# Kernel optimization log

Hardware: AMD Instinct MI355X
Metric: run time of the kernel (lower is better)

Reference implementation:

```python
import jax, jax.numpy as jnp
import numpy as np

EPS = 1e-5
K = 20

def knn(x, k):
    # x: (B, 3, N) -> idx (B, N, k) of nearest neighbors (negative sq-dist topk)
    inner = -2.0 * jnp.einsum('bcn,bcm->bnm', x, x)
    xx = jnp.sum(x * x, axis=1)  # (B, N)
    pd = -xx[:, :, None] - inner - xx[:, None, :]
    return jax.lax.top_k(pd, k)[1]

def graph_feature(feats, idx):
    # feats: (B, C, N), idx: (B, N, k) -> (B, 2C, N, k)
    ft = jnp.transpose(feats, (0, 2, 1))  # (B, N, C)
    gathered = jax.vmap(lambda f, i: f[i])(ft, idx)  # (B, N, k, C)
    center = ft[:, :, None, :]  # (B, N, 1, C)
    out = jnp.concatenate([gathered - center,
                           jnp.broadcast_to(center, gathered.shape)], axis=3)
    return jnp.transpose(out, (0, 3, 1, 2))  # (B, 2C, N, k)

def bn2d(h, g, b):
    m = jnp.mean(h, axis=(0, 2, 3), keepdims=True)
    v = jnp.var(h, axis=(0, 2, 3), keepdims=True)
    return (h - m) * jax.lax.rsqrt(v + EPS) * g[None, :, None, None] + b[None, :, None, None]

def bn1d(h, g, b):
    m = jnp.mean(h, axis=(0, 2), keepdims=True)
    v = jnp.var(h, axis=(0, 2), keepdims=True)
    return (h - m) * jax.lax.rsqrt(v + EPS) * g[None, :, None] + b[None, :, None]

def edge_block(x, feats, w, g, b):
    idx = knn(x, K)
    ef = graph_feature(feats, idx)                  # (B, 2C, N, k)
    h = jnp.einsum('bcnk,oc->bonk', ef, w)          # 1x1 conv, no bias
    h = jnp.tanh(bn2d(h, g, b))
    return jnp.max(h, axis=-1)                      # (B, O, N)


def setup_inputs() -> dict:
    key = jax.random.key(0)
    ks = jax.random.split(key, 20)
    B, N, FD, EMB = 8, 2048, 3, 1024
    def w_init(k, o, i):
        return jax.random.normal(k, (o, i), dtype=jnp.float32) * (1.0 / np.sqrt(i))
    inp = {
        'x': jax.random.normal(ks[0], (B, N, 3), dtype=jnp.float32),
        'features': jax.random.normal(ks[1], (B, N, FD), dtype=jnp.float32),
        'w1': w_init(ks[2], 64, 2 * FD),
        'g1': jnp.ones((64,), jnp.float32), 'b1': jnp.zeros((64,), jnp.float32),
        'w2': w_init(ks[3], 64, 128),
        'g2': jnp.ones((64,), jnp.float32), 'b2': jnp.zeros((64,), jnp.float32),
        'w3': w_init(ks[4], 128, 128),
        'g3': jnp.ones((128,), jnp.float32), 'b3': jnp.zeros((128,), jnp.float32),
        'w4': w_init(ks[5], 256, 256),
        'g4': jnp.ones((256,), jnp.float32), 'b4': jnp.zeros((256,), jnp.float32),
        'w5': w_init(ks[6], EMB, 512),
        'g5': jnp.ones((EMB,), jnp.float32), 'b5': jnp.zeros((EMB,), jnp.float32),
    }
    return inp


def reference(x, features, w1, g1, b1, w2, g2, b2, w3, g3, b3, w4, g4, b4, w5, g5, b5):
    xt = jnp.transpose(x, (0, 2, 1))          # (B, 3, N)
    ft = jnp.transpose(features, (0, 2, 1))   # (B, FD, N)
    B = xt.shape[0]
    f1 = edge_block(xt, ft, w1, g1, b1)       # (B, 64, N)
    f2 = edge_block(xt, f1, w2, g2, b2)       # (B, 64, N)
    f3 = edge_block(xt, f2, w3, g3, b3)       # (B, 128, N)
    f4 = edge_block(xt, f3, w4, g4, b4)       # (B, 256, N)
    cat = jnp.concatenate([f1, f2, f3, f4], axis=1)   # (B, 512, N)
    f5 = jnp.tanh(bn1d(jnp.einsum('bcn,oc->bon', cat, w5), g5, b5))  # (B, EMB, N)
    mx = jnp.max(f5, axis=-1)
    av = jnp.mean(f5, axis=-1)
    return jnp.concatenate([mx, av], axis=1)  # (B, 2*EMB)
```

## Files before the change

kernel.cpp:

```cpp
#include <hip/hip_runtime.h>
#include <cstdio>
#include <cstdint>

#define NPTS 2048
#define NB   8
#define KK   20

typedef __attribute__((ext_vector_type(8))) short  short8;
typedef __attribute__((ext_vector_type(8))) unsigned short ushort8;
typedef __attribute__((ext_vector_type(4))) float  f32x4;
typedef unsigned short ushort;
typedef unsigned int   uint;

#define AS1 __attribute__((address_space(1)))
#define AS3 __attribute__((address_space(3)))

__device__ __forceinline__ ushort f2bf(float f) {
    uint u = __float_as_uint(f);
    u += 0x7fffu + ((u >> 16) & 1u);
    return (ushort)(u >> 16);
}
__device__ __forceinline__ float bf2f(ushort s) { return __uint_as_float((uint)s << 16); }

__device__ __forceinline__ void gload16(const ushort* g, ushort* l) {
    __builtin_amdgcn_global_load_lds((const AS1 uint*)(const void*)g,
                                     (AS3 uint*)(void*)l, 16, 0, 0);
}

__global__ __launch_bounds__(256) void knn_kernel(const float* __restrict__ x,
                                                  int* __restrict__ idx)
{
    __shared__ float4 sp[NPTS];
    const int tid = threadIdx.x;
    const int wv = tid >> 6, lane = tid & 63;
    const int gn0 = blockIdx.x * 4;
    const int b = gn0 >> 11;
    const float* xb = x + (size_t)b * NPTS * 3;

    for (int p = tid; p < NPTS; p += 256) {
        const float a0 = xb[p * 3 + 0], a1 = xb[p * 3 + 1], a2 = xb[p * 3 + 2];
        sp[p] = make_float4(a0, a1, a2, a0 * a0 + a1 * a1 + a2 * a2);
    }
    __syncthreads();

    const int n = (gn0 & (NPTS - 1)) + wv;
    const float4 pn = sp[n];
    const float xxn = pn.w;

    float d[32];
#pragma unroll
    for (int i = 0; i < 32; ++i) {
        const float4 pm = sp[lane + i * 64];
        const float dot = pm.x * pn.x + pm.y * pn.y + pm.z * pn.z;
        const float inner = -2.0f * dot;
        d[i] = (-xxn - inner) - pm.w;
    }

    int* op = idx + ((size_t)b * NPTS + n) * KK;
    for (int it = 0; it < KK; ++it) {
        float bv = -1e38f;
        int   bi = 0;
#pragma unroll
        for (int i = 0; i < 32; ++i) {
            const bool better = d[i] > bv;
            bv = better ? d[i] : bv;
            bi = better ? (lane + i * 64) : bi;
        }
#pragma unroll
        for (int s = 32; s; s >>= 1) {
            const float ov = __shfl_xor(bv, s);
            const int   oi = __shfl_xor(bi, s);
            const bool better = (ov > bv) || (ov == bv && oi < bi);
            bv = better ? ov : bv;
            bi = better ? oi : bi;
        }
        if (lane == 0) op[it] = bi;
#pragma unroll
        for (int i = 0; i < 32; ++i)
            if (bi == lane + i * 64) d[i] = -1e38f;
    }
}

__global__ __launch_bounds__(256) void y1_kernel(const float* __restrict__ feats,
                                                 const float* __restrict__ w1,
                                                 float* __restrict__ Y)
{
    __shared__ float w[384];
    const int tid = threadIdx.x;
    for (int i = tid; i < 384; i += 256) w[i] = w1[i];
    __syncthreads();

    const int b  = blockIdx.y;
    const int p  = blockIdx.x * 2 + (tid >> 7);
    const int o2 = tid & 127;
    const int o = o2 & 63, half = o2 >> 6;
    const float* fp = feats + ((size_t)b * NPTS + p) * 3;
    const float f0 = fp[0], f1 = fp[1], f2 = fp[2];
    const float* wr = &w[o * 6 + half * 3];
    Y[((size_t)b * NPTS + p) * 128 + o2] = wr[0] * f0 + wr[1] * f1 + wr[2] * f2;
}

__global__ __launch_bounds__(256) void wsplit_kernel(const float* __restrict__ w2,
                                                     const float* __restrict__ w3,
                                                     const float* __restrict__ w4,
                                                     ushort* q2h, ushort* q2l,
                                                     ushort* q3h, ushort* q3l,
                                                     ushort* q4h, ushort* q4l)
{
    const int t = blockIdx.x * 256 + threadIdx.x;
    float v; ushort *dh, *dl; int off;
    if (t < 8192)        { int i = t;         int m = i >> 6, c = i & 63;  int o = m & 63,  hf = m >> 6; v = w2[o * 128 + hf * 64  + c]; dh = q2h; dl = q2l; off = i; }
    else if (t < 24576)  { int i = t - 8192;  int m = i >> 6, c = i & 63;  int o = m & 127, hf = m >> 7; v = w3[o * 128 + hf * 64  + c]; dh = q3h; dl = q3l; off = i; }
    else if (t < 90112)  { int i = t - 24576; int m = i >> 7, c = i & 127; int o = m & 255, hf = m >> 8; v = w4[o * 256 + hf * 128 + c]; dh = q4h; dl = q4l; off = i; }
    else return;
    const ushort h = f2bf(v);
    dh[off] = h;
    dl[off] = f2bf(v - bf2f(h));
}

template<bool PF32>
__global__ __launch_bounds__(256) void gemm_mfma(const float* __restrict__ Pf,
                                                 const ushort* __restrict__ Ph,
                                                 const ushort* __restrict__ Pl,
                                                 const ushort* __restrict__ Qh,
                                                 const ushort* __restrict__ Ql,
                                                 float* __restrict__ Out,
                                                 int K, int pitchP, int pitchQ, int ldO,
                                                 long strideP, long strideQ, long strideO)
{
    constexpr int PH = 0, PL = 8192, QH = 16384, QL = 24576;
    __shared__ ushort lds_buf[32768];

    const int tid  = threadIdx.x;
    const int wv   = tid >> 6, lane = tid & 63;
    const int i0   = blockIdx.x * 128;
    const int j0   = blockIdx.y * 128;
    const long prow0 = (long)blockIdx.z * strideP + (long)i0 * pitchP;
    const long qrow0 = (long)blockIdx.z * strideQ + (long)j0 * pitchQ;

    const int iw = (wv >> 1) * 64;
    const int jw = (wv & 1) * 64;
    const int lr = lane & 15;
    const int lc = lane >> 4;

    f32x4 acc[4][4];
#pragma unroll
    for (int f = 0; f < 4; ++f)
#pragma unroll
        for (int g = 0; g < 4; ++g) acc[f][g] = (f32x4){0.f, 0.f, 0.f, 0.f};

    for (int k0 = 0; k0 < K; k0 += 64) {
        __syncthreads();
        {
            const int r8 = lane >> 3;
            const int cp = lane & 7;
#pragma unroll
            for (int q = 0; q < 4; ++q) {
                const int row = wv * 32 + q * 8 + r8;
                const int cl  = cp ^ (row & 7);
                const long go = (long)row * pitchQ + k0 + cl * 8;
                gload16(Qh + qrow0 + go, &lds_buf[QH + (wv * 32 + q * 8) * 64]);
                gload16(Ql + qrow0 + go, &lds_buf[QL + (wv * 32 + q * 8) * 64]);
            }
        }
        if constexpr (!PF32) {
            const int r8 = lane >> 3;
            const int cp = lane & 7;
#pragma unroll
            for (int q = 0; q < 4; ++q) {
                const int row = wv * 32 + q * 8 + r8;
                const int cl  = cp ^ (row & 7);
                const long go = (long)row * pitchP + k0 + cl * 8;
                gload16(Ph + prow0 + go, &lds_buf[PH + (wv * 32 + q * 8) * 64]);
                gload16(Pl + prow0 + go, &lds_buf[PL + (wv * 32 + q * 8) * 64]);
            }
        } else {
#pragma unroll
            for (int r = 0; r < 4; ++r) {
                const int id  = r * 256 + tid;
                const int row = id >> 3, cl = id & 7;
                const int cp  = cl ^ (row & 7);
                const float* gp = Pf + prow0 + (long)row * pitchP + k0 + cl * 8;
                const float4 v0 = *(const float4*)gp;
                const float4 v1 = *(const float4*)(gp + 4);
                const float vv[8] = {v0.x, v0.y, v0.z, v0.w, v1.x, v1.y, v1.z, v1.w};
                ushort8 hi, lo;
#pragma unroll
                for (int e2 = 0; e2 < 8; ++e2) {
                    const ushort h = f2bf(vv[e2]);
                    hi[e2] = h;
                    lo[e2] = f2bf(vv[e2] - bf2f(h));
                }
                *(ushort8*)&lds_buf[PH + row * 64 + cp * 8] = hi;
                *(ushort8*)&lds_buf[PL + row * 64 + cp * 8] = lo;
            }
        }
        asm volatile("s_waitcnt vmcnt(0)" ::: "memory");
        __syncthreads();

#pragma unroll
        for (int kk = 0; kk < 2; ++kk) {
            const int cpa = (kk * 4 + lc) ^ (lr & 7);
            short8 ah[4], al[4], bh[4], bl[4];
#pragma unroll
            for (int f = 0; f < 4; ++f) {
                const int ra = (iw + f * 16 + lr) * 64 + cpa * 8;
                ah[f] = *(const short8*)&lds_buf[PH + ra];
                al[f] = *(const short8*)&lds_buf[PL + ra];
                const int rb = (jw + f * 16 + lr) * 64 + cpa * 8;
                bh[f] = *(const short8*)&lds_buf[QH + rb];
                bl[f] = *(const short8*)&lds_buf[QL + rb];
            }
#pragma unroll
            for (int f = 0; f < 4; ++f)
#pragma unroll
                for (int g = 0; g < 4; ++g) {
                    acc[f][g] = __builtin_amdgcn_mfma_f32_16x16x32_bf16(ah[f], bh[g], acc[f][g], 0, 0, 0);
                    acc[f][g] = __builtin_amdgcn_mfma_f32_16x16x32_bf16(ah[f], bl[g], acc[f][g], 0, 0, 0);
                    acc[f][g] = __builtin_amdgcn_mfma_f32_16x16x32_bf16(al[f], bh[g], acc[f][g], 0, 0, 0);
                }
        }
    }

    const long ob = (long)blockIdx.z * strideO;
#pragma unroll
    for (int f = 0; f < 4; ++f) {
        const int i = i0 + iw + f * 16 + lc * 4;
#pragma unroll
        for (int g = 0; g < 4; ++g) {
            const int j = j0 + jw + g * 16 + lr;
#pragma unroll
            for (int r = 0; r < 4; ++r)
                Out[ob + (long)(i + r) * ldO + j] = acc[f][g][r];
        }
    }
}

template<int O, int NCH>
__global__ __launch_bounds__(256) void edge_apply(const float* __restrict__ Y,
                                                  const int* __restrict__ knn_idx,
                                                  float* __restrict__ mx_out,
                                                  double* __restrict__ st)
{
    constexpr int M = 2 * O;
    constexpr int NPB = 256 / O;
    const int b   = blockIdx.y;
    const int tid = threadIdx.x;
    const int o   = tid & (O - 1);
    const int sub = tid / O;
    const int n0  = blockIdx.x * (NPB * NCH);
    const size_t rowb = (size_t)b * NPTS;
    float s = 0.f, s2 = 0.f;

#pragma unroll
    for (int it = 0; it < NCH; ++it) {
        const int n = n0 + it * NPB + sub;
        const float* yr = Y + (rowb + n) * M;
        const float base = yr[O + o] - yr[o];
        const int* ip = knn_idx + (rowb + n) * KK;
        int mm[KK];
#pragma unroll
        for (int j = 0; j < KK; ++j) mm[j] = ip[j];
        float h[KK];
#pragma unroll
        for (int j = 0; j < KK; ++j) h[j] = Y[(rowb + mm[j]) * M + o];
        float mx = -1e38f;
#pragma unroll
        for (int j = 0; j < KK; ++j) {
            const float v = h[j] + base;
            mx = fmaxf(mx, v);
            s += v;
            s2 = fmaf(v, v, s2);
        }
        mx_out[(rowb + n) * O + o] = mx;
    }
    double* stp = st + (size_t)(blockIdx.x & 7) * (2 * O);
    atomicAdd(&stp[o],     (double)s);
    atomicAdd(&stp[O + o], (double)s2);
}

template<int O>
__global__ __launch_bounds__(256) void edge_finalize(const float* __restrict__ mx_in,
                                                     const double* __restrict__ st,
                                                     const float* __restrict__ gamma,
                                                     const float* __restrict__ beta,
                                                     ushort* __restrict__ ch,
                                                     ushort* __restrict__ cl_,
                                                     int c0)
{
    __shared__ float ssc[256], ssh[256];
    const int b = blockIdx.y;
    const int tid = threadIdx.x;
    if (tid < O) {
        double ssum = 0.0, s2sum = 0.0;
#pragma unroll
        for (int sl = 0; sl < 8; ++sl) {
            ssum  += st[(size_t)sl * (2 * O) + tid];
            s2sum += st[(size_t)sl * (2 * O) + O + tid];
        }
        const double cnt = (double)NB * NPTS * KK;
        const double mean = ssum / cnt;
        const double var  = s2sum / cnt - mean * mean;
        const float rs = rsqrtf((float)var + 1e-5f);
        const float sc = gamma[tid] * rs;
        ssc[tid] = sc;
        ssh[tid] = beta[tid] - (float)mean * sc;
    }
    __syncthreads();

    const int o   = tid & (O - 1);
    const int sub = tid / O;
    const int n0  = blockIdx.x * 8;
    constexpr int NPB = 256 / O;
#pragma unroll
    for (int it = 0; it < 8 / NPB; ++it) {
        const int n = n0 + it * NPB + sub;
        const float v = mx_in[((size_t)b * NPTS + n) * O + o];
        const float f = tanhf(fmaf(v, ssc[o], ssh[o]));
        const ushort h = f2bf(f);
        const size_t co = ((size_t)b * NPTS + n) * 512 + c0 + o;
        ch[co]  = h;
        cl_[co] = f2bf(f - bf2f(h));
    }
}

__global__ __launch_bounds__(256) void estats_kernel(const float* __restrict__ e,
                                                     double* __restrict__ st)
{
    const int o = blockIdx.x;
    const int tid = threadIdx.x;
    double s = 0.0, s2 = 0.0;
    for (int b = 0; b < NB; ++b) {
        const float* row = e + ((size_t)(b * 1024 + o)) * NPTS;
        for (int n = tid; n < NPTS; n += 256) {
            const float v = row[n];
            s  += v;
            s2 += (double)v * v;
        }
    }
    __shared__ double sh_s[4], sh_s2[4];
#pragma unroll
    for (int d = 32; d > 0; d >>= 1) { s += __shfl_xor(s, d); s2 += __shfl_xor(s2, d); }
    const int lane = tid & 63, wv = tid >> 6;
    if (lane == 0) { sh_s[wv] = s; sh_s2[wv] = s2; }
    __syncthreads();
    if (tid == 0) {
        st[o]        = sh_s[0] + sh_s[1] + sh_s[2] + sh_s[3];
        st[1024 + o] = sh_s2[0] + sh_s2[1] + sh_s2[2] + sh_s2[3];
    }
}

__global__ __launch_bounds__(256) void final_kernel(const float* __restrict__ e,
                                                    const double* __restrict__ st,
                                                    const float* __restrict__ g5,
                                                    const float* __restrict__ b5,
                                                    float* __restrict__ out)
{
    const int b = blockIdx.y;
    const int wv = threadIdx.x >> 6, lane = threadIdx.x & 63;
    const int o = blockIdx.x * 4 + wv;
    const double cnt = (double)NB * NPTS;
    const double mean = st[o] / cnt;
    const double var  = st[1024 + o] / cnt - mean * mean;
    const float rs = rsqrtf((float)var + 1e-5f);
    const float sc = g5[o] * rs;
    const float sh = b5[o] - (float)mean * sc;
    const float* row = e + ((size_t)(b * 1024 + o)) * NPTS;
    float mx = -1e38f, sm = 0.f;
    for (int n = lane; n < NPTS; n += 64) {
        const float v = tanhf(fmaf(row[n], sc, sh));
        mx = fmaxf(mx, v);
        sm += v;
    }
#pragma unroll
    for (int d = 32; d > 0; d >>= 1) {
        mx = fmaxf(mx, __shfl_xor(mx, d));
        sm += __shfl_xor(sm, d);
    }
    if (lane == 0) {
        out[(size_t)b * 2048 + o]        = mx;
        out[(size_t)b * 2048 + 1024 + o] = sm * (1.0f / 2048.0f);
    }
}

extern "C" void kernel_launch(void* const* d_in, const int* in_sizes, int n_in,
                              void* d_out, int out_size, void* d_ws, size_t ws_size,
                              hipStream_t stream)
{
    (void)in_sizes; (void)n_in; (void)out_size;
    const float* x  = (const float*)d_in[0];
    const float* ft = (const float*)d_in[1];
    const float* w1 = (const float*)d_in[2];
    const float* g1 = (const float*)d_in[3];
    const float* b1 = (const float*)d_in[4];
    const float* w2 = (const float*)d_in[5];
    const float* g2 = (const float*)d_in[6];
    const float* b2 = (const float*)d_in[7];
    const float* w3 = (const float*)d_in[8];
    const float* g3 = (const float*)d_in[9];
    const float* b3 = (const float*)d_in[10];
    const float* w4 = (const float*)d_in[11];
    const float* g4 = (const float*)d_in[12];
    const float* b4 = (const float*)d_in[13];
    const float* w5 = (const float*)d_in[14];
    const float* g5 = (const float*)d_in[15];
    const float* b5 = (const float*)d_in[16];
    float* out = (float*)d_out;

    const size_t STATS_OFF = 0;
    const size_t ESTAT_OFF = 131072;
    const size_t IDX_OFF   = 147456;
    const size_t Q2H_OFF   = 1458176,  Q2L_OFF = 1474560;
    const size_t Q3H_OFF   = 1490944,  Q3L_OFF = 1523712;
    const size_t Q4H_OFF   = 1556480,  Q4L_OFF = 1687552;
    const size_t CTH_OFF   = 1835008;
    const size_t CTL_OFF   = 18612224;
    const size_t Y_OFF     = 35389440;
    const size_t MX_OFF    = 68943872;
    const size_t NEED      = 102498304;
    if (ws_size < NEED) {
        fprintf(stderr, "kernel_launch: ws too small (%zu < %zu)\n", ws_size, NEED);
        return;
    }
    char* ws = (char*)d_ws;
    double* stats  = (double*)(ws + STATS_OFF);
    double* estats = (double*)(ws + ESTAT_OFF);
    int*    idx    = (int*)(ws + IDX_OFF);
    ushort* q2h = (ushort*)(ws + Q2H_OFF); ushort* q2l = (ushort*)(ws + Q2L_OFF);
    ushort* q3h = (ushort*)(ws + Q3H_OFF); ushort* q3l = (ushort*)(ws + Q3L_OFF);
    ushort* q4h = (ushort*)(ws + Q4H_OFF); ushort* q4l = (ushort*)(ws + Q4L_OFF);
    ushort* cth = (ushort*)(ws + CTH_OFF); ushort* ctl = (ushort*)(ws + CTL_OFF);
    float*  Y   = (float*)(ws + Y_OFF);
    float*  mxb = (float*)(ws + MX_OFF);
    float*  e   = (float*)(ws + Y_OFF);

    hipMemsetAsync(stats, 0, 131072, stream);

    knn_kernel<<<NB * NPTS / 4, 256, 0, stream>>>(x, idx);
    wsplit_kernel<<<352, 256, 0, stream>>>(w2, w3, w4, q2h, q2l, q3h, q3l, q4h, q4l);

    y1_kernel<<<dim3(NPTS / 2, NB), 256, 0, stream>>>(ft, w1, Y);
    edge_apply<64, 2><<<dim3(256, NB), 256, 0, stream>>>(Y, idx, mxb, stats + 0 * 4096);
    edge_finalize<64><<<dim3(256, NB), 256, 0, stream>>>(mxb, stats + 0 * 4096, g1, b1, cth, ctl, 0);

    gemm_mfma<false><<<dim3(16, 1, 8), 256, 0, stream>>>(
        nullptr, cth + 0, ctl + 0, q2h, q2l, Y,
        64, 512, 64, 128, (long)NPTS * 512, 0, (long)NPTS * 128);
    edge_apply<64, 2><<<dim3(256, NB), 256, 0, stream>>>(Y, idx, mxb, stats + 1 * 4096);
    edge_finalize<64><<<dim3(256, NB), 256, 0, stream>>>(mxb, stats + 1 * 4096, g2, b2, cth, ctl, 64);

    gemm_mfma<false><<<dim3(16, 2, 8), 256, 0, stream>>>(
        nullptr, cth + 64, ctl + 64, q3h, q3l, Y,
        64, 512, 64, 256, (long)NPTS * 512, 0, (long)NPTS * 256);
    edge_apply<128, 4><<<dim3(256, NB), 256, 0, stream>>>(Y, idx, mxb, stats + 2 * 4096);
    edge_finalize<128><<<dim3(256, NB), 256, 0, stream>>>(mxb, stats + 2 * 4096, g3, b3, cth, ctl, 128);

    gemm_mfma<false><<<dim3(16, 4, 8), 256, 0, stream>>>(
        nullptr, cth + 128, ctl + 128, q4h, q4l, Y,
        128, 512, 128, 512, (long)NPTS * 512, 0, (long)NPTS * 512);
    edge_apply<256, 8><<<dim3(256, NB), 256, 0, stream>>>(Y, idx, mxb, stats + 3 * 4096);
    edge_finalize<256><<<dim3(256, NB), 256, 0, stream>>>(mxb, stats + 3 * 4096, g4, b4, cth, ctl, 256);

    gemm_mfma<true><<<dim3(8, 16, 8), 256, 0, stream>>>(
        w5, nullptr, nullptr, cth, ctl, e,
        512, 512, 512, 2048, 0, (long)NPTS * 512, (long)1024 * 2048);
    estats_kernel<<<1024, 256, 0, stream>>>(e, estats);
    final_kernel<<<dim3(256, NB), 256, 0, stream>>>(e, estats, g5, b5, out);
}
```

Baseline: 469.6 us.

## Speed up kNN top-k with grouped maxima and packed-key wave reduction

The kNN selection now keeps a per-lane maximum for each of four groups of eight candidates and recomputes only the winning group after each pick, instead of rescanning all 32 distances every iteration. The cross-lane reduction packs the order-preserving float bits and the inverted index into one 64-bit key, so a single shuffle chain replaces the separate value and index shuffles. The kNN block grows to 512 threads (8 queries per block) to amortise the shared-memory point load. Separately, edge_apply uses a flat grid that interleaves batches across consecutive blocks, which spreads the Y gathers across batches and changes which atomic stat slot each block hits.

```diff
diff --git a/kernel.cpp b/kernel.cpp
--- a/kernel.cpp
+++ b/kernel.cpp
@@ -27,17 +27,17 @@
                                      (AS3 uint*)(void*)l, 16, 0, 0);
 }
 
-__global__ __launch_bounds__(256) void knn_kernel(const float* __restrict__ x,
+__global__ __launch_bounds__(512) void knn_kernel(const float* __restrict__ x,
                                                   int* __restrict__ idx)
 {
     __shared__ float4 sp[NPTS];
     const int tid = threadIdx.x;
     const int wv = tid >> 6, lane = tid & 63;
-    const int gn0 = blockIdx.x * 4;
+    const int gn0 = blockIdx.x * 8;
     const int b = gn0 >> 11;
     const float* xb = x + (size_t)b * NPTS * 3;
 
-    for (int p = tid; p < NPTS; p += 256) {
+    for (int p = tid; p < NPTS; p += 512) {
         const float a0 = xb[p * 3 + 0], a1 = xb[p * 3 + 1], a2 = xb[p * 3 + 2];
         sp[p] = make_float4(a0, a1, a2, a0 * a0 + a1 * a1 + a2 * a2);
     }
@@ -56,28 +56,57 @@
         d[i] = (-xxn - inner) - pm.w;
     }
 
+    float gv[4]; int gs[4];
+#pragma unroll
+    for (int g = 0; g < 4; ++g) {
+        float v = d[g * 8]; int s = 0;
+#pragma unroll
+        for (int j = 1; j < 8; ++j)
+            if (d[g * 8 + j] > v) { v = d[g * 8 + j]; s = j; }
+        gv[g] = v; gs[g] = s;
+    }
+
     int* op = idx + ((size_t)b * NPTS + n) * KK;
     for (int it = 0; it < KK; ++it) {
-        float bv = -1e38f;
-        int   bi = 0;
-#pragma unroll
-        for (int i = 0; i < 32; ++i) {
-            const bool better = d[i] > bv;
-            bv = better ? d[i] : bv;
-            bi = better ? (lane + i * 64) : bi;
-        }
-#pragma unroll
-        for (int s = 32; s; s >>= 1) {
-            const float ov = __shfl_xor(bv, s);
-            const int   oi = __shfl_xor(bi, s);
-            const bool better = (ov > bv) || (ov == bv && oi < bi);
-            bv = better ? ov : bv;
-            bi = better ? oi : bi;
-        }
-        if (lane == 0) op[it] = bi;
-#pragma unroll
-        for (int i = 0; i < 32; ++i)
-            if (bi == lane + i * 64) d[i] = -1e38f;
+        float bv = gv[0]; int bm8 = gs[0];
+#pragma unroll
+        for (int g = 1; g < 4; ++g)
+            if (gv[g] > bv) { bv = gv[g]; bm8 = g * 8 + gs[g]; }
+        const int m = lane + (bm8 << 6);
+
+        const uint u = __float_as_uint(bv);
+        const uint r = (u & 0x80000000u) ? ~u : (u | 0x80000000u);
+        unsigned long long key =
+            ((unsigned long long)r << 11) | (unsigned)(2047 - m);
+
+#pragma unroll
+        for (int s2 = 32; s2; s2 >>= 1) {
+            const unsigned long long ok =
+                (unsigned long long)__shfl_xor((long long)key, s2);
+            key = (ok > key) ? ok : key;
+        }
+        const int mw = 2047 - (int)(key & 2047u);
+        if (lane == 0) op[it] = mw;
+
+        const int mws   = __builtin_amdgcn_readfirstlane(mw);
+        const int wslot = mws >> 6;
+        const int wgrp  = wslot >> 3;
+        const int wj    = wslot & 7;
+        const bool iswin = (lane == (mws & 63));
+
+#pragma unroll
+        for (int G = 0; G < 4; ++G) {
+            if (wgrp == G) {
+#pragma unroll
+                for (int j = 0; j < 8; ++j)
+                    if (j == wj) d[G * 8 + j] = iswin ? -1e38f : d[G * 8 + j];
+                float v = d[G * 8]; int s = 0;
+#pragma unroll
+                for (int j = 1; j < 8; ++j)
+                    if (d[G * 8 + j] > v) { v = d[G * 8 + j]; s = j; }
+                gv[G] = v; gs[G] = s;
+            }
+        }
     }
 }
 
@@ -244,11 +273,13 @@
 {
     constexpr int M = 2 * O;
     constexpr int NPB = 256 / O;
-    const int b   = blockIdx.y;
+    const int blk = blockIdx.x;
+    const int b     = blk & 7;
+    const int chunk = blk >> 3;
     const int tid = threadIdx.x;
     const int o   = tid & (O - 1);
     const int sub = tid / O;
-    const int n0  = blockIdx.x * (NPB * NCH);
+    const int n0  = chunk * (NPB * NCH);
     const size_t rowb = (size_t)b * NPTS;
     float s = 0.f, s2 = 0.f;
 
@@ -274,7 +305,7 @@
         }
         mx_out[(rowb + n) * O + o] = mx;
     }
-    double* stp = st + (size_t)(blockIdx.x & 7) * (2 * O);
+    double* stp = st + (size_t)(chunk & 7) * (2 * O);
     atomicAdd(&stp[o],     (double)s);
     atomicAdd(&stp[O + o], (double)s2);
 }
@@ -436,29 +467,29 @@
 
     hipMemsetAsync(stats, 0, 131072, stream);
 
-    knn_kernel<<<NB * NPTS / 4, 256, 0, stream>>>(x, idx);
+    knn_kernel<<<NB * NPTS / 8, 512, 0, stream>>>(x, idx);
     wsplit_kernel<<<352, 256, 0, stream>>>(w2, w3, w4, q2h, q2l, q3h, q3l, q4h, q4l);
 
     y1_kernel<<<dim3(NPTS / 2, NB), 256, 0, stream>>>(ft, w1, Y);
-    edge_apply<64, 2><<<dim3(256, NB), 256, 0, stream>>>(Y, idx, mxb, stats + 0 * 4096);
+    edge_apply<64, 2><<<2048, 256, 0, stream>>>(Y, idx, mxb, stats + 0 * 4096);
     edge_finalize<64><<<dim3(256, NB), 256, 0, stream>>>(mxb, stats + 0 * 4096, g1, b1, cth, ctl, 0);
 
     gemm_mfma<false><<<dim3(16, 1, 8), 256, 0, stream>>>(
         nullptr, cth + 0, ctl + 0, q2h, q2l, Y,
         64, 512, 64, 128, (long)NPTS * 512, 0, (long)NPTS * 128);
-    edge_apply<64, 2><<<dim3(256, NB), 256, 0, stream>>>(Y, idx, mxb, stats + 1 * 4096);
+    edge_apply<64, 2><<<2048, 256, 0, stream>>>(Y, idx, mxb, stats + 1 * 4096);
     edge_finalize<64><<<dim3(256, NB), 256, 0, stream>>>(mxb, stats + 1 * 4096, g2, b2, cth, ctl, 64);
 
     gemm_mfma<false><<<dim3(16, 2, 8), 256, 0, stream>>>(
         nullptr, cth + 64, ctl + 64, q3h, q3l, Y,
         64, 512, 64, 256, (long)NPTS * 512, 0, (long)NPTS * 256);
-    edge_apply<128, 4><<<dim3(256, NB), 256, 0, stream>>>(Y, idx, mxb, stats + 2 * 4096);
+    edge_apply<128, 4><<<2048, 256, 0, stream>>>(Y, idx, mxb, stats + 2 * 4096);
     edge_finalize<128><<<dim3(256, NB), 256, 0, stream>>>(mxb, stats + 2 * 4096, g3, b3, cth, ctl, 128);
 
     gemm_mfma<false><<<dim3(16, 4, 8), 256, 0, stream>>>(
         nullptr, cth + 128, ctl + 128, q4h, q4l, Y,
         128, 512, 128, 512, (long)NPTS * 512, 0, (long)NPTS * 512);
-    edge_apply<256, 8><<<dim3(256, NB), 256, 0, stream>>>(Y, idx, mxb, stats + 3 * 4096);
+    edge_apply<256, 8><<<2048, 256, 0, stream>>>(Y, idx, mxb, stats + 3 * 4096);
     edge_finalize<256><<<dim3(256, NB), 256, 0, stream>>>(mxb, stats + 3 * 4096, g4, b4, cth, ctl, 256);
 
     gemm_mfma<true><<<dim3(8, 16, 8), 256, 0, stream>>>(
```

Measured after the change: 400.7 us. 14.7% less time.
